# Kernel tuning notes

Measured on AMD Instinct MI355X. Metric: run time of the kernel, lower is better.

## Reference

```python
import jax, jax.numpy as jnp
import numpy as np

B, CH, H, W, D = 2, 32, 256, 512, 192


def setup_inputs() -> dict:
    key = jax.random.key(0)
    ks = jax.random.split(key, 10)
    def w(k, shape, fan_in):
        return jax.random.normal(k, shape, jnp.float32) * (1.0 / np.sqrt(fan_in))
    return {
        "x": jax.random.normal(ks[0], (B, CH, H, W), jnp.float32),
        "y": jax.random.normal(ks[1], (B, CH, H, W), jnp.float32),
        # encoder: 1x1 convs ch->64->32->1 (shared for x and y)
        "w1": w(ks[2], (64, CH), CH), "b1": w(ks[3], (64,), CH),
        "w2": w(ks[4], (32, 64), 64), "b2": w(ks[5], (32,), 64),
        "w3": w(ks[6], (1, 32), 32), "b3": w(ks[7], (1,), 32),
        # decoderl: 1x1 conv maxdisp->maxdisp (original code applies decoderl to BOTH volumes)
        "wd": w(ks[8], (D, D), D), "bd": w(ks[9], (D,), D),
    }


def _conv1x1(w, b, h):  # [O,C] x [B,C,H,W] -> [B,O,H,W]
    return jnp.einsum("oc,bchw->bohw", w, h) + b[None, :, None, None]


def _encoder(x, w1, b1, w2, b2, w3, b3):
    h = jax.nn.relu(x)
    h = jax.nn.relu(_conv1x1(w1, b1, h))
    h = jax.nn.relu(_conv1x1(w2, b2, h))
    h = jax.nn.relu(_conv1x1(w3, b3, h))
    return h[:, 0]  # squeeze channel -> [B,H,W]


def _cost_volumes(xf, yf):
    # costx[b,d,h,w] = xf[b,h,w+d] * yf[b,h,w]   (0 where w+d >= W)
    # costy[b,d,h,w] = xf[b,h,w]   * yf[b,h,w-d] (0 where w-d < 0)
    dgrid = jnp.arange(D)
    wgrid = jnp.arange(W)
    x_pad = jnp.pad(xf, ((0, 0), (0, 0), (0, D)))          # zero pad right
    xg = x_pad[:, :, wgrid[None, :] + dgrid[:, None]]       # [B,H,D,W]
    costx = (xg * yf[:, :, None, :]).transpose(0, 2, 1, 3)  # [B,D,H,W]
    y_pad = jnp.pad(yf, ((0, 0), (0, 0), (D, 0)))           # zero pad left
    yg = y_pad[:, :, wgrid[None, :] - dgrid[:, None] + D]   # [B,H,D,W]
    costy = (xf[:, :, None, :] * yg).transpose(0, 2, 1, 3)  # [B,D,H,W]
    return costx, costy


def reference(x, y, w1, b1, w2, b2, w3, b3, wd, bd):
    xf = _encoder(x, w1, b1, w2, b2, w3, b3)
    yf = _encoder(y, w1, b1, w2, b2, w3, b3)
    costx, costy = _cost_volumes(xf, yf)
    probx = jax.nn.softmax(_conv1x1(wd, bd, costx), axis=1)
    proby = jax.nn.softmax(_conv1x1(wd, bd, costy), axis=1)  # decoderl used for both, as in source
    disp_vals = jnp.arange(D, dtype=probx.dtype)
    dispx = jnp.einsum("bdhw,d->bhw", probx, disp_vals)
    dispy = jnp.einsum("bdhw,d->bhw", proby, disp_vals)
    return dispx, dispy
```

## Files before the change

### kernel.cpp

```cpp
#include <hip/hip_runtime.h>


typedef __attribute__((ext_vector_type(8)))  __bf16 bf16x8;
typedef __attribute__((ext_vector_type(4)))  float  f32x4;
typedef __attribute__((ext_vector_type(16))) float  f32x16;

#define MFMA32(a,b,c) __builtin_amdgcn_mfma_f32_32x32x16_bf16((a),(b),(c),0,0,0)
#define MFMA16(a,b,c) __builtin_amdgcn_mfma_f32_16x16x32_bf16((a),(b),(c),0,0,0)

constexpr int WW  = 512;
constexpr int HW  = 256 * 512;
constexpr int CHW = 32 * HW;
constexpr float LOG2E = 1.4426950408889634f;

constexpr size_t XFB_OFF = 0;
constexpr int    STB     = 25600;
constexpr size_t WDP_OFF = 2 * 262144 * 2;
constexpr size_t BDP_OFF = WDP_OFF + 3 * STB;

__global__ __launch_bounds__(512)
void panet_encode(const float* __restrict__ gx,  const float* __restrict__ gy,
                  const float* __restrict__ gw1, const float* __restrict__ gb1,
                  const float* __restrict__ gw2, const float* __restrict__ gb2,
                  const float* __restrict__ gw3, const float* __restrict__ gb3,
                  const float* __restrict__ gwd, const float* __restrict__ gbd,
                  char* __restrict__ ws)
{
  const int blk = blockIdx.x;
  const int tid = threadIdx.x;

  if (blk >= 1024) {
    const int pi = blk - 1024;
    unsigned short* wdp = (unsigned short*)(ws + WDP_OFF);
    for (int idx = tid; idx < 12 * 200; idx += 512) {
      const int oo = idx / 200;
      const int k  = idx - oo * 200;
      const int o  = 12 * pi + oo;
      const int stage = o >> 6;
      const int r     = o & 63;
      unsigned short v = 0;
      if (k < 192) v = __builtin_bit_cast(unsigned short, (__bf16)gwd[o * 192 + k]);
      wdp[stage * 12800 + r * 200 + k] = v;
    }
    if (pi == 0) {
      float* bdp = (float*)(ws + BDP_OFF);
      if (tid < 192) bdp[tid] = gbd[tid] * LOG2E;
    }
    return;
  }

  const int t    = blk >> 9;
  const int bh   = blk & 511;
  const int lane = tid & 63;
  const int m    = lane & 15;
  const int g    = lane >> 4;
  const int wid  = tid >> 6;

  bf16x8 A1[4], A2[2][2];
  f32x4  bias1[4], bias2[2], w3v[2];
  #pragma unroll
  for (int Mt = 0; Mt < 4; ++Mt) {
    const float* p = gw1 + (16 * Mt + m) * 32 + 4 * g;
    const f32x4 u0 = *(const f32x4*)p;
    const f32x4 u1 = *(const f32x4*)(p + 16);
    #pragma unroll
    for (int j = 0; j < 4; ++j) { A1[Mt][j] = (__bf16)u0[j]; A1[Mt][j + 4] = (__bf16)u1[j]; }
    bias1[Mt] = *(const f32x4*)(gb1 + 16 * Mt + 4 * g);
  }
  #pragma unroll
  for (int Mt = 0; Mt < 2; ++Mt) {
    #pragma unroll
    for (int s = 0; s < 2; ++s) {
      const float* p = gw2 + (16 * Mt + m) * 64 + 32 * s + 4 * g;
      const f32x4 u0 = *(const f32x4*)p;
      const f32x4 u1 = *(const f32x4*)(p + 16);
      #pragma unroll
      for (int j = 0; j < 4; ++j) { A2[Mt][s][j] = (__bf16)u0[j]; A2[Mt][s][j + 4] = (__bf16)u1[j]; }
    }
    bias2[Mt] = *(const f32x4*)(gb2 + 16 * Mt + 4 * g);
    w3v[Mt]   = *(const f32x4*)(gw3 + 16 * Mt + 4 * g);
  }
  const float b3s = gb3[0];
  const f32x4 zf4 = {0.f, 0.f, 0.f, 0.f};
  const float* base = (t ? gy : gx) + (bh >> 8) * CHW + (bh & 255) * WW;
  unsigned short* xfb = (unsigned short*)(ws + XFB_OFF) + t * 262144 + bh * 512;

  for (int u = wid; u < 32; u += 8) {
    const int w0 = u << 4;
    const float* src = base + w0 + m;

    bf16x8 B1;
    #pragma unroll
    for (int j = 0; j < 8; ++j) {
      const int c = 16 * (j >> 2) + 4 * g + (j & 3);
      B1[j] = (__bf16)fmaxf(src[c * HW], 0.f);
    }
    f32x4 acc1[4];
    #pragma unroll
    for (int Mt = 0; Mt < 4; ++Mt) acc1[Mt] = MFMA16(A1[Mt], B1, zf4);

    bf16x8 B2[2];
    #pragma unroll
    for (int s = 0; s < 2; ++s) {
      #pragma unroll
      for (int j = 0; j < 4; ++j) {
        B2[s][j]     = (__bf16)fmaxf(acc1[2 * s][j]     + bias1[2 * s][j],     0.f);
        B2[s][j + 4] = (__bf16)fmaxf(acc1[2 * s + 1][j] + bias1[2 * s + 1][j], 0.f);
      }
    }
    f32x4 acc2[2];
    #pragma unroll
    for (int Mt = 0; Mt < 2; ++Mt)
      acc2[Mt] = MFMA16(A2[Mt][1], B2[1], MFMA16(A2[Mt][0], B2[0], zf4));

    float s3 = 0.f;
    #pragma unroll
    for (int Mt = 0; Mt < 2; ++Mt)
      #pragma unroll
      for (int r = 0; r < 4; ++r)
        s3 += w3v[Mt][r] * fmaxf(acc2[Mt][r] + bias2[Mt][r], 0.f);
    s3 += __shfl_xor(s3, 16);
    s3 += __shfl_xor(s3, 32);
    const float val = fmaxf(s3 + b3s, 0.f);

    if (lane < 16)
      xfb[w0 + m] = __builtin_bit_cast(unsigned short, (__bf16)val);
  }
}

constexpr int CPS    = 1424;
constexpr int K2_WD  = 0;
constexpr int K2_HK  = STB;
constexpr int K2_BD  = K2_HK + 11392;
constexpr int K2_LDS = K2_BD + 768;

__global__ __launch_bounds__(256)
void panet_corr(const char* __restrict__ ws, float* __restrict__ gout)
{
  __shared__ __align__(16) char lds[K2_LDS];
  const int blk  = blockIdx.x;
  const int dir  = blk >> 10;
  const int bh   = (blk >> 1) & 511;
  const int ch2  = blk & 1;
  const int tid  = threadIdx.x;
  const int lane = tid & 63;
  const int l31  = lane & 31;
  const int h    = lane >> 5;
  const int wid  = tid >> 6;

  const unsigned short* xfb = (const unsigned short*)(ws + XFB_OFF);
  const unsigned short* hs = xfb + (dir ? 262144 : 0) + bh * 512;
  const unsigned short* ss = xfb + (dir ? 0 : 262144) + bh * 512;

  f32x4 streg[7];

  {
    const char* src = ws + WDP_OFF;
    #pragma unroll
    for (int k = 0; k < 6; ++k) streg[k] = *(const f32x4*)(src + (tid + 256 * k) * 16);
    if (tid < 64) streg[6] = *(const f32x4*)(src + (tid + 1536) * 16);

    int* zp = (int*)(lds + K2_HK);
    for (int i = tid; i < 11392 / 4; i += 256) zp[i] = 0;
    const float* bdp = (const float*)(ws + BDP_OFF);
    if (tid < 192) ((float*)(lds + K2_BD))[tid] = bdp[tid];
  }
  __syncthreads();
  #pragma unroll
  for (int e0 = 0; e0 < 512; e0 += 256) {
    const int e = e0 + tid;
    #pragma unroll
    for (int c = 0; c < 8; ++c) {
      if (e + c <= 511)
        ((unsigned short*)(lds + K2_HK + c * CPS))[e] = hs[dir ? (511 - e - c) : (e + c)];
    }
  }
  {
    char* dst = lds + K2_WD;
    #pragma unroll
    for (int k = 0; k < 6; ++k) *(f32x4*)(dst + (tid + 256 * k) * 16) = streg[k];
    if (tid < 64) *(f32x4*)(dst + (tid + 1536) * 16) = streg[6];
    const char* src = ws + WDP_OFF + STB;
    #pragma unroll
    for (int k = 0; k < 6; ++k) streg[k] = *(const f32x4*)(src + (tid + 256 * k) * 16);
    if (tid < 64) streg[6] = *(const f32x4*)(src + (tid + 1536) * 16);
  }
  __syncthreads();

  int bfb[2]; float sc[2];
  #pragma unroll
  for (int ct = 0; ct < 2; ++ct) {
    const int col = ch2 * 256 + wid * 64 + ct * 32 + l31;
    const int I0  = dir ? (511 - col) : col;
    const int cc  = I0 & 7;
    bfb[ct] = K2_HK + cc * CPS + 2 * (I0 - cc) + 16 * h;
    sc[ct]  = LOG2E * __builtin_bit_cast(float, (unsigned)ss[col] << 16);
  }
  const int baseA = l31 * 400 + 16 * h;

  float stM[2] = {-3.4e38f, -3.4e38f};
  float stS[2] = {0.f, 0.f};
  float stW[2] = {0.f, 0.f};

  for (int s = 0; s < 3; ++s) {
    f32x16 a00 = {0}, a01 = {0}, a10 = {0}, a11 = {0};
    #pragma unroll 2
    for (int ks = 0; ks < 12; ++ks) {
      const int ko = 32 * ks;
      const bf16x8 af0 = *(const bf16x8*)(lds + K2_WD + baseA + ko);
      const bf16x8 af1 = *(const bf16x8*)(lds + K2_WD + baseA + 12800 + ko);
      const bf16x8 bf0 = *(const bf16x8*)(lds + bfb[0] + ko);
      const bf16x8 bf1 = *(const bf16x8*)(lds + bfb[1] + ko);
      a00 = MFMA32(af0, bf0, a00);
      a01 = MFMA32(af0, bf1, a01);
      a10 = MFMA32(af1, bf0, a10);
      a11 = MFMA32(af1, bf1, a11);
    }

    #pragma unroll
    for (int ct = 0; ct < 2; ++ct) {
      const f32x16 A0 = ct ? a01 : a00;
      const f32x16 A1 = ct ? a11 : a10;
      float L0[16], L1[16];
      #pragma unroll
      for (int q = 0; q < 4; ++q) {
        const f32x4 bd0 = *(const f32x4*)(lds + K2_BD + (64 * s + 8 * q + 4 * h) * 4);
        const f32x4 bd1 = *(const f32x4*)(lds + K2_BD + (64 * s + 8 * q + 4 * h + 32) * 4);
        #pragma unroll
        for (int r = 0; r < 4; ++r) {
          L0[4 * q + r] = fmaf(sc[ct], A0[4 * q + r], bd0[r]);
          L1[4 * q + r] = fmaf(sc[ct], A1[4 * q + r], bd1[r]);
        }
      }
      float t[16];
      #pragma unroll
      for (int i = 0; i < 16; ++i) t[i] = fmaxf(L0[i], L1[i]);
      #pragma unroll
      for (int off = 8; off > 0; off >>= 1)
        #pragma unroll
        for (int i = 0; i < off; ++i) t[i] = fmaxf(t[i], t[i + off]);
      const float nm   = fmaxf(stM[ct], t[0]);
      const float fold = __builtin_amdgcn_exp2f(stM[ct] - nm);
      float lsp[4] = {0.f, 0.f, 0.f, 0.f}, lwp[4] = {0.f, 0.f, 0.f, 0.f};
      #pragma unroll
      for (int i = 0; i < 16; ++i) {
        const float c  = (float)((i & 3) + 8 * (i >> 2));
        const float p0 = __builtin_amdgcn_exp2f(L0[i] - nm);
        const float p1 = __builtin_amdgcn_exp2f(L1[i] - nm);
        lsp[i & 3] += p0 + p1;
        lwp[i & 3] = fmaf(c, p0, lwp[i & 3]);
        lwp[i & 3] = fmaf(c + 32.f, p1, lwp[i & 3]);
      }
      float ls = (lsp[0] + lsp[1]) + (lsp[2] + lsp[3]);
      float lw = (lwp[0] + lwp[1]) + (lwp[2] + lwp[3]);
      lw = fmaf((float)(64 * s + 4 * h), ls, lw);
      stS[ct] = fmaf(stS[ct], fold, ls);
      stW[ct] = fmaf(stW[ct], fold, lw);
      stM[ct] = nm;
    }

    if (s < 2) {
      __syncthreads();
      char* dst = lds + K2_WD;
      #pragma unroll
      for (int k = 0; k < 6; ++k) *(f32x4*)(dst + (tid + 256 * k) * 16) = streg[k];
      if (tid < 64) *(f32x4*)(dst + (tid + 1536) * 16) = streg[6];
      if (s == 0) {
        const char* src = ws + WDP_OFF + 2 * STB;
        #pragma unroll
        for (int k = 0; k < 6; ++k) streg[k] = *(const f32x4*)(src + (tid + 256 * k) * 16);
        if (tid < 64) streg[6] = *(const f32x4*)(src + (tid + 1536) * 16);
      }
      __syncthreads();
    }
  }

  float* outp = gout + dir * 262144 + bh * 512 + ch2 * 256;
  #pragma unroll
  for (int ct = 0; ct < 2; ++ct) {
    const float Mo = __shfl_xor(stM[ct], 32);
    const float M  = fmaxf(stM[ct], Mo);
    const float f  = __builtin_amdgcn_exp2f(stM[ct] - M);
    float sr = stS[ct] * f;
    float wr = stW[ct] * f;
    sr += __shfl_xor(sr, 32);
    wr += __shfl_xor(wr, 32);
    if (lane < 32) outp[wid * 64 + ct * 32 + l31] = wr / sr;
  }
}

extern "C" void kernel_launch(void* const* d_in, const int* in_sizes, int n_in,
                              void* d_out, int out_size, void* d_ws, size_t ws_size,
                              hipStream_t stream) {
  const float* x  = (const float*)d_in[0];
  const float* y  = (const float*)d_in[1];
  const float* w1 = (const float*)d_in[2];
  const float* b1 = (const float*)d_in[3];
  const float* w2 = (const float*)d_in[4];
  const float* b2 = (const float*)d_in[5];
  const float* w3 = (const float*)d_in[6];
  const float* b3 = (const float*)d_in[7];
  const float* wd = (const float*)d_in[8];
  const float* bd = (const float*)d_in[9];
  char* ws = (char*)d_ws;

  panet_encode<<<1040, 512, 0, stream>>>(x, y, w1, b1, w2, b2, w3, b3, wd, bd, ws);
  panet_corr<<<2048, 256, 0, stream>>>(ws, (float*)d_out);
}
```

Measured before the change: 80.33 us.

## Drop LDS staging in corr kernel; read pre-laid-out weights and shifted features from global

The encoder now writes each feature row a second time into a padded global buffer holding two parity-shifted copies, so the correlation kernel can load MFMA B fragments straight from global with 4-byte-aligned vector loads. The decoder weights are repacked into an MFMA-fragment-friendly layout that is also read directly from global. This removes all shared-memory staging, zero-fill and block barriers from the correlation kernel. In exchange, every MFMA operand now comes from L1/L2 instead of LDS, and the encoder does extra scattered 2-byte stores.

```diff
diff --git a/kernel.cpp b/kernel.cpp
--- a/kernel.cpp
+++ b/kernel.cpp
@@ -2,6 +2,7 @@
 
 
 typedef __attribute__((ext_vector_type(8)))  __bf16 bf16x8;
+typedef __attribute__((ext_vector_type(8), aligned(4))) __bf16 bf16x8u;
 typedef __attribute__((ext_vector_type(4)))  float  f32x4;
 typedef __attribute__((ext_vector_type(16))) float  f32x16;
 
@@ -14,9 +15,11 @@
 constexpr float LOG2E = 1.4426950408889634f;
 
 constexpr size_t XFB_OFF = 0;
-constexpr int    STB     = 25600;
-constexpr size_t WDP_OFF = 2 * 262144 * 2;
-constexpr size_t BDP_OFF = WDP_OFF + 3 * STB;
+constexpr size_t HKG_OFF = 1048576;
+constexpr int    HRP     = 2848;
+constexpr size_t HDP     = 512ull * HRP;
+constexpr size_t PA_OFF  = HKG_OFF + 2 * HDP;
+constexpr size_t BDP_OFF = PA_OFF + 73728;
 
 __global__ __launch_bounds__(512)
 void panet_encode(const float* __restrict__ gx,  const float* __restrict__ gy,
@@ -31,17 +34,24 @@
 
   if (blk >= 1024) {
     const int pi = blk - 1024;
-    unsigned short* wdp = (unsigned short*)(ws + WDP_OFF);
-    for (int idx = tid; idx < 12 * 200; idx += 512) {
-      const int oo = idx / 200;
-      const int k  = idx - oo * 200;
-      const int o  = 12 * pi + oo;
-      const int stage = o >> 6;
-      const int r     = o & 63;
-      unsigned short v = 0;
-      if (k < 192) v = __builtin_bit_cast(unsigned short, (__bf16)gwd[o * 192 + k]);
-      wdp[stage * 12800 + r * 200 + k] = v;
-    }
+    char* pab = ws + PA_OFF;
+    for (int idx = tid; idx < 12 * 192; idx += 512) {
+      const int rr = idx / 192;
+      const int rem = idx - rr * 192;
+      const int kw = rem >> 3;
+      const int j  = rem & 7;
+      const int row = 12 * pi + rr;
+      const __bf16 v = (__bf16)gwd[row * 192 + 8 * kw + j];
+      ((unsigned short*)(pab + (kw * 192 + row) * 16))[j] =
+          __builtin_bit_cast(unsigned short, v);
+    }
+    unsigned short* hkb = (unsigned short*)(ws + HKG_OFF);
+    for (int d = 0; d < 2; ++d)
+      for (int rr = 0; rr < 32; ++rr) {
+        unsigned short* hk = hkb + d * (HDP / 2) + (size_t)(32 * pi + rr) * (HRP / 2);
+        for (int e = 512 + tid; e < 712; e += 512) hk[e] = 0;
+        for (int e = 511 + tid; e < 712; e += 512) hk[712 + e] = 0;
+      }
     if (pi == 0) {
       float* bdp = (float*)(ws + BDP_OFF);
       if (tid < 192) bdp[tid] = gbd[tid] * LOG2E;
@@ -84,6 +94,7 @@
   const f32x4 zf4 = {0.f, 0.f, 0.f, 0.f};
   const float* base = (t ? gy : gx) + (bh >> 8) * CHW + (bh & 255) * WW;
   unsigned short* xfb = (unsigned short*)(ws + XFB_OFF) + t * 262144 + bh * 512;
+  unsigned short* hk  = (unsigned short*)(ws + HKG_OFF) + t * (HDP / 2) + (size_t)bh * (HRP / 2);
 
   for (int u = wid; u < 32; u += 8) {
     const int w0 = u << 4;
@@ -123,21 +134,24 @@
     s3 += __shfl_xor(s3, 32);
     const float val = fmaxf(s3 + b3s, 0.f);
 
-    if (lane < 16)
-      xfb[w0 + m] = __builtin_bit_cast(unsigned short, (__bf16)val);
+    if (lane < 16) {
+      const int px = w0 + m;
+      const unsigned short bits = __builtin_bit_cast(unsigned short, (__bf16)val);
+      xfb[px] = bits;
+      if (t == 0) {
+        hk[px] = bits;
+        if (px >= 1) hk[712 + px - 1] = bits;
+      } else {
+        hk[511 - px] = bits;
+        if (px <= 510) hk[712 + 510 - px] = bits;
+      }
+    }
   }
 }
-
-constexpr int CPS    = 1424;
-constexpr int K2_WD  = 0;
-constexpr int K2_HK  = STB;
-constexpr int K2_BD  = K2_HK + 11392;
-constexpr int K2_LDS = K2_BD + 768;
 
 __global__ __launch_bounds__(256)
 void panet_corr(const char* __restrict__ ws, float* __restrict__ gout)
 {
-  __shared__ __align__(16) char lds[K2_LDS];
   const int blk  = blockIdx.x;
   const int dir  = blk >> 10;
   const int bh   = (blk >> 1) & 511;
@@ -148,55 +162,21 @@
   const int h    = lane >> 5;
   const int wid  = tid >> 6;
 
-  const unsigned short* xfb = (const unsigned short*)(ws + XFB_OFF);
-  const unsigned short* hs = xfb + (dir ? 262144 : 0) + bh * 512;
-  const unsigned short* ss = xfb + (dir ? 0 : 262144) + bh * 512;
-
-  f32x4 streg[7];
-
-  {
-    const char* src = ws + WDP_OFF;
-    #pragma unroll
-    for (int k = 0; k < 6; ++k) streg[k] = *(const f32x4*)(src + (tid + 256 * k) * 16);
-    if (tid < 64) streg[6] = *(const f32x4*)(src + (tid + 1536) * 16);
-
-    int* zp = (int*)(lds + K2_HK);
-    for (int i = tid; i < 11392 / 4; i += 256) zp[i] = 0;
-    const float* bdp = (const float*)(ws + BDP_OFF);
-    if (tid < 192) ((float*)(lds + K2_BD))[tid] = bdp[tid];
-  }
-  __syncthreads();
-  #pragma unroll
-  for (int e0 = 0; e0 < 512; e0 += 256) {
-    const int e = e0 + tid;
-    #pragma unroll
-    for (int c = 0; c < 8; ++c) {
-      if (e + c <= 511)
-        ((unsigned short*)(lds + K2_HK + c * CPS))[e] = hs[dir ? (511 - e - c) : (e + c)];
-    }
-  }
-  {
-    char* dst = lds + K2_WD;
-    #pragma unroll
-    for (int k = 0; k < 6; ++k) *(f32x4*)(dst + (tid + 256 * k) * 16) = streg[k];
-    if (tid < 64) *(f32x4*)(dst + (tid + 1536) * 16) = streg[6];
-    const char* src = ws + WDP_OFF + STB;
-    #pragma unroll
-    for (int k = 0; k < 6; ++k) streg[k] = *(const f32x4*)(src + (tid + 256 * k) * 16);
-    if (tid < 64) streg[6] = *(const f32x4*)(src + (tid + 1536) * 16);
-  }
-  __syncthreads();
-
-  int bfb[2]; float sc[2];
+  const unsigned short* xfbu = (const unsigned short*)(ws + XFB_OFF);
+  const unsigned short* ss = xfbu + (dir ? 0 : 262144) + bh * 512;
+  const char* hkrow = ws + HKG_OFF + dir * HDP + (size_t)bh * HRP;
+  const char* pa    = ws + PA_OFF;
+  const float* bdp  = (const float*)(ws + BDP_OFF);
+
+  const char* bptr[2]; float sc[2];
   #pragma unroll
   for (int ct = 0; ct < 2; ++ct) {
     const int col = ch2 * 256 + wid * 64 + ct * 32 + l31;
     const int I0  = dir ? (511 - col) : col;
-    const int cc  = I0 & 7;
-    bfb[ct] = K2_HK + cc * CPS + 2 * (I0 - cc) + 16 * h;
+    const int p   = I0 & 1;
+    bptr[ct] = hkrow + p * 1424 + 2 * (I0 - p) + 16 * h;
     sc[ct]  = LOG2E * __builtin_bit_cast(float, (unsigned)ss[col] << 16);
   }
-  const int baseA = l31 * 400 + 16 * h;
 
   float stM[2] = {-3.4e38f, -3.4e38f};
   float stS[2] = {0.f, 0.f};
@@ -204,13 +184,13 @@
 
   for (int s = 0; s < 3; ++s) {
     f32x16 a00 = {0}, a01 = {0}, a10 = {0}, a11 = {0};
+    const char* abase = pa + (h * 192 + 64 * s + l31) * 16;
     #pragma unroll 2
     for (int ks = 0; ks < 12; ++ks) {
-      const int ko = 32 * ks;
-      const bf16x8 af0 = *(const bf16x8*)(lds + K2_WD + baseA + ko);
-      const bf16x8 af1 = *(const bf16x8*)(lds + K2_WD + baseA + 12800 + ko);
-      const bf16x8 bf0 = *(const bf16x8*)(lds + bfb[0] + ko);
-      const bf16x8 bf1 = *(const bf16x8*)(lds + bfb[1] + ko);
+      const bf16x8 af0 = __builtin_bit_cast(bf16x8, *(const bf16x8u*)(abase + ks * 6144));
+      const bf16x8 af1 = __builtin_bit_cast(bf16x8, *(const bf16x8u*)(abase + ks * 6144 + 512));
+      const bf16x8 bf0 = __builtin_bit_cast(bf16x8, *(const bf16x8u*)(bptr[0] + 32 * ks));
+      const bf16x8 bf1 = __builtin_bit_cast(bf16x8, *(const bf16x8u*)(bptr[1] + 32 * ks));
       a00 = MFMA32(af0, bf0, a00);
       a01 = MFMA32(af0, bf1, a01);
       a10 = MFMA32(af1, bf0, a10);
@@ -224,8 +204,8 @@
       float L0[16], L1[16];
       #pragma unroll
       for (int q = 0; q < 4; ++q) {
-        const f32x4 bd0 = *(const f32x4*)(lds + K2_BD + (64 * s + 8 * q + 4 * h) * 4);
-        const f32x4 bd1 = *(const f32x4*)(lds + K2_BD + (64 * s + 8 * q + 4 * h + 32) * 4);
+        const f32x4 bd0 = *(const f32x4*)(bdp + 64 * s + 8 * q + 4 * h);
+        const f32x4 bd1 = *(const f32x4*)(bdp + 64 * s + 8 * q + 4 * h + 32);
         #pragma unroll
         for (int r = 0; r < 4; ++r) {
           L0[4 * q + r] = fmaf(sc[ct], A0[4 * q + r], bd0[r]);
@@ -257,21 +237,6 @@
       stS[ct] = fmaf(stS[ct], fold, ls);
       stW[ct] = fmaf(stW[ct], fold, lw);
       stM[ct] = nm;
-    }
-
-    if (s < 2) {
-      __syncthreads();
-      char* dst = lds + K2_WD;
-      #pragma unroll
-      for (int k = 0; k < 6; ++k) *(f32x4*)(dst + (tid + 256 * k) * 16) = streg[k];
-      if (tid < 64) *(f32x4*)(dst + (tid + 1536) * 16) = streg[6];
-      if (s == 0) {
-        const char* src = ws + WDP_OFF + 2 * STB;
-        #pragma unroll
-        for (int k = 0; k < 6; ++k) streg[k] = *(const f32x4*)(src + (tid + 256 * k) * 16);
-        if (tid < 64) streg[6] = *(const f32x4*)(src + (tid + 1536) * 16);
-      }
-      __syncthreads();
     }
   }
 
```

New measurement: 101.9 us. 1.27x slower.
